# Kernel optimization log

Hardware: AMD Instinct MI355X
Metric: run time of the kernel (lower is better)

Reference implementation:

```python
import jax, jax.numpy as jnp
import numpy as np

B, L, SIZE, BACK, H = 4, 1024, 1024, 512, 16
D = SIZE // H  # head_size = 64


def setup_inputs() -> dict:
    key = jax.random.key(0)
    ks = jax.random.split(key, 18)
    s = 0.02
    return {
        "k": jax.random.normal(ks[0], (B, L, SIZE), jnp.float32),
        "v": jax.random.normal(ks[1], (B, L, SIZE), jnp.float32),
        "q": jax.random.normal(ks[2], (B, L, SIZE), jnp.float32),
        "background": jax.random.normal(ks[3], (B, L, BACK), jnp.float32),
        # weights stored [in, out] (pre-transposed vs torch Linear)
        "Wk": jax.random.normal(ks[4], (SIZE, SIZE), jnp.float32) * s,
        "bk": jnp.zeros((SIZE,), jnp.float32),
        "Wv": jax.random.normal(ks[5], (SIZE, SIZE), jnp.float32) * s,
        "bv": jnp.zeros((SIZE,), jnp.float32),
        "Wq": jax.random.normal(ks[6], (SIZE, SIZE), jnp.float32) * s,
        "bq": jnp.zeros((SIZE,), jnp.float32),
        "Wb": jax.random.normal(ks[7], (BACK, SIZE), jnp.float32) * s,
        "bb": jnp.zeros((SIZE,), jnp.float32),
        "Wo": jax.random.normal(ks[8], (SIZE, SIZE), jnp.float32) * s,
        "bo": jnp.zeros((SIZE,), jnp.float32),
    }


def _heads(x):
    # [B, L, H*D] -> [B, H, L, D]
    b, l, _ = x.shape
    return x.reshape(b, l, H, D).transpose(0, 2, 1, 3)


def reference(k, v, q, background, Wk, bk, Wv, bv, Wq, bq, Wb, bb, Wo, bo):
    kh = _heads(k @ Wk + bk)
    vh = _heads(v @ Wv + bv)
    qh = _heads(q @ Wq + bq) / jnp.sqrt(jnp.asarray(D, k.dtype))
    gh = _heads(background @ Wb + bb)
    scores = jnp.einsum("bhqd,bhkd->bhqk", qh, kh)   # [B,H,Lq,Lk]
    gates = jax.nn.sigmoid(jnp.einsum("bhqd,bhkd->bhqk", qh, gh))
    attn = jax.nn.softmax(scores, axis=-1) * gates    # dropout = identity (eval)
    ctx = jnp.einsum("bhqk,bhkd->bhqd", attn, vh)
    ctx = ctx.transpose(0, 2, 1, 3).reshape(k.shape[0], -1, H * D)
    return ctx @ Wo + bo
```

## Files before the change

### kernel.cpp

```cpp
#include <hip/hip_runtime.h>
#include <cstddef>
#include <cstdint>

typedef __attribute__((ext_vector_type(8))) short s16x8;
typedef __attribute__((ext_vector_type(4))) short s16x4;
typedef __attribute__((ext_vector_type(4))) float f32x4;
typedef __attribute__((ext_vector_type(4))) unsigned u32x4;

#define MFMA(a, b, c) __builtin_amdgcn_mfma_f32_16x16x32_bf16(a, b, c, 0, 0, 0)
#define LOG2E 1.44269504088896f

__device__ __forceinline__ short f2bf(float x) {
    uint32_t u = __float_as_uint(x);
    u = (u + 0x7FFFu + ((u >> 16) & 1u)) >> 16;
    return (short)u;
}

__device__ __forceinline__ void gld16(const void* g, void* l) {
    __builtin_amdgcn_global_load_lds(
        (const __attribute__((address_space(1))) unsigned int*)g,
        (__attribute__((address_space(3))) unsigned int*)l, 16, 0, 0);
}

__device__ __forceinline__ float fexp2(float x) {
#if __has_builtin(__builtin_amdgcn_exp2f)
    return __builtin_amdgcn_exp2f(x);
#else
    return exp2f(x);
#endif
}

__device__ __forceinline__ float frcp(float x) {
#if __has_builtin(__builtin_amdgcn_rcpf)
    return __builtin_amdgcn_rcpf(x);
#else
    return 1.f / x;
#endif
}

__device__ __forceinline__ unsigned cvtpk(float lo, float hi) {
    unsigned r;
    asm("v_cvt_pk_bf16_f32 %0, %1, %2" : "=v"(r) : "v"(lo), "v"(hi));
    return r;
}

struct WtP { const float* W[5]; short* Wt[5]; int K[5]; };

__global__ __launch_bounds__(256)
void conv_wt_b(WtP p) {
    __shared__ float T[64][65];
    const int z = blockIdx.z;
    const int K = p.K[z];
    const int k0 = blockIdx.y << 6, n0 = blockIdx.x << 6;
    if (k0 >= K) return;
    const float* W = p.W[z];
    short* Wt = p.Wt[z];
    const int tr = threadIdx.x >> 4, tc4 = (threadIdx.x & 15) << 2;
    #pragma unroll
    for (int i = 0; i < 4; ++i) {
        const int r = tr + i * 16;
        const float4 v = *(const float4*)(W + (size_t)(k0 + r) * 1024 + n0 + tc4);
        T[r][tc4 + 0] = v.x; T[r][tc4 + 1] = v.y;
        T[r][tc4 + 2] = v.z; T[r][tc4 + 3] = v.w;
    }
    __syncthreads();
    #pragma unroll
    for (int i = 0; i < 4; ++i) {
        const int nr = tr + i * 16;
        s16x4 o;
        o[0] = f2bf(T[tc4 + 0][nr]); o[1] = f2bf(T[tc4 + 1][nr]);
        o[2] = f2bf(T[tc4 + 2][nr]); o[3] = f2bf(T[tc4 + 3][nr]);
        *(s16x4*)(Wt + (size_t)(n0 + nr) * K + k0 + tc4) = o;
    }
}

struct Proj5P {
    const float* Af[5];
    const short* A[5];
    const short* Bt[5]; const float* bias[5];
    void* Y[5]; int Kd[5]; float alpha[5]; int mode[5];
};

__global__ __launch_bounds__(256, 2)
void proj_gemm128f(Proj5P p) {
    __shared__ __align__(16) short lds[2 * 16384];

    const int tid = threadIdx.x;
    const int w = tid >> 6, lane = tid & 63;
    const int la = lane & 15, kg = lane >> 4;
    const int wr = w >> 1, wc = w & 1;

    const int orig = blockIdx.x;
    const int swz = (orig & 7) * 128 + (orig >> 3);
    const int z = swz >> 8;
    const int rem = swz & 255;
    const int bm = rem >> 3, bn = rem & 7;

    const int K = p.Kd[z];
    const int NT = K >> 6;

    const int srow = tid >> 3;
    const int csrc = (tid & 7) ^ (srow & 7);
    const float* gAf = p.Af[z] + (size_t)(bm * 128 + srow) * K + csrc * 8;
    const short* gB  = p.Bt[z] + (size_t)(bn * 128 + srow) * K + csrc * 8;
    short* dstA = &lds[srow * 64 + (tid & 7) * 8];
    short* dstB = dstA + 8192;

    float4 av[4][2];

#define ISSUE_A(t) do {                                                    \
        const size_t ko_ = (size_t)((t) << 6);                             \
        _Pragma("unroll")                                                  \
        for (int i = 0; i < 4; ++i) {                                      \
            av[i][0] = *(const float4*)(gAf + (size_t)(32 * i) * K + ko_);     \
            av[i][1] = *(const float4*)(gAf + (size_t)(32 * i) * K + ko_ + 4); \
        }                                                                  \
    } while (0)
#define ISSUE_B(t, nb) do {                                                \
        const size_t ko_ = (size_t)((t) << 6);                             \
        _Pragma("unroll")                                                  \
        for (int i = 0; i < 4; ++i)                                        \
            gld16(gB + (size_t)(32 * i) * K + ko_,                         \
                  dstB + (nb) * 16384 + i * 2048);                         \
    } while (0)
#define A_WRITE(nb) do {                                                   \
        _Pragma("unroll")                                                  \
        for (int i = 0; i < 4; ++i) {                                      \
            u32x4 pk;                                                      \
            pk[0] = cvtpk(av[i][0].x, av[i][0].y);                         \
            pk[1] = cvtpk(av[i][0].z, av[i][0].w);                         \
            pk[2] = cvtpk(av[i][1].x, av[i][1].y);                         \
            pk[3] = cvtpk(av[i][1].z, av[i][1].w);                         \
            *(u32x4*)(dstA + (nb) * 16384 + i * 2048) = pk;                \
        }                                                                  \
    } while (0)

    const int c0 = kg ^ (la & 7), c1 = (4 + kg) ^ (la & 7);
    const int aRd = (wr * 64 + la) * 64;
    const int bRd = 8192 + (wc * 64 + la) * 64;

    f32x4 acc[4][4] = {};

    ISSUE_A(0);
    ISSUE_B(0, 0);
    A_WRITE(0);
    asm volatile("s_waitcnt vmcnt(0) lgkmcnt(0)" ::: "memory");
    asm volatile("s_barrier" ::: "memory");
    ISSUE_A(1);

    for (int t = 0; t < NT; ++t) {
        const int cb = (t & 1) * 16384;
        const int nbi = (t & 1) ^ 1;
        if (t + 1 < NT) ISSUE_B(t + 1, nbi);
        s16x8 af[4][2], bf[4][2];
        #pragma unroll
        for (int m = 0; m < 4; ++m) {
            af[m][0] = *(const s16x8*)&lds[cb + aRd + m * 1024 + c0 * 8];
            af[m][1] = *(const s16x8*)&lds[cb + aRd + m * 1024 + c1 * 8];
        }
        #pragma unroll
        for (int n = 0; n < 4; ++n) {
            bf[n][0] = *(const s16x8*)&lds[cb + bRd + n * 1024 + c0 * 8];
            bf[n][1] = *(const s16x8*)&lds[cb + bRd + n * 1024 + c1 * 8];
        }
        __builtin_amdgcn_s_setprio(1);
        #pragma unroll
        for (int m = 0; m < 4; ++m)
            #pragma unroll
            for (int n = 0; n < 4; ++n) {
                acc[m][n] = MFMA(af[m][0], bf[n][0], acc[m][n]);
                acc[m][n] = MFMA(af[m][1], bf[n][1], acc[m][n]);
            }
        __builtin_amdgcn_s_setprio(0);
        if (t + 1 < NT) {
            A_WRITE(nbi);
            if (t + 2 < NT) {
                ISSUE_A(t + 2);
                asm volatile("s_waitcnt vmcnt(8)" ::: "memory");
            } else {
                asm volatile("s_waitcnt vmcnt(0)" ::: "memory");
            }
            asm volatile("s_waitcnt lgkmcnt(0)" ::: "memory");
            asm volatile("s_barrier" ::: "memory");
        }
    }
#undef ISSUE_A
#undef ISSUE_B
#undef A_WRITE

    const float* __restrict__ bias = p.bias[z];
    const float alpha = p.alpha[z];
    const int mode = p.mode[z];

    if (mode == 2) {
        short* __restrict__ Y = (short*)p.Y[z];
        short* Tv = lds;
        asm volatile("s_waitcnt lgkmcnt(0)" ::: "memory");
        asm volatile("s_barrier" ::: "memory");
        #pragma unroll
        for (int ni = 0; ni < 4; ++ni) {
            const int rrow = wc * 64 + ni * 16 + la;
            const float bs = bias[bn * 128 + rrow];
            #pragma unroll
            for (int mi = 0; mi < 4; ++mi) {
                const int l0 = wr * 64 + mi * 16 + kg * 4;
                const unsigned d0 = cvtpk(alpha * (acc[mi][ni][0] + bs),
                                          alpha * (acc[mi][ni][1] + bs));
                const unsigned d1 = cvtpk(alpha * (acc[mi][ni][2] + bs),
                                          alpha * (acc[mi][ni][3] + bs));
                *(unsigned*)&Tv[rrow * 132 + l0]     = d0;
                *(unsigned*)&Tv[rrow * 132 + l0 + 2] = d1;
            }
        }
        asm volatile("s_waitcnt lgkmcnt(0)" ::: "memory");
        asm volatile("s_barrier" ::: "memory");
        const int bb_ = (bm * 128) >> 10;
        const int l0g = (bm * 128) & 1023;
        #pragma unroll
        for (int s = 0; s < 8; ++s) {
            const int c = tid + (s << 8);
            const int rr = c >> 4, seg = c & 15;
            const int hh = bn * 2 + (rr >> 6), dd = rr & 63;
            const s16x8 vv = *(const s16x8*)&Tv[rr * 132 + seg * 8];
            *(s16x8*)&Y[((((size_t)bb_ * 16 + hh) * 64 + dd) << 10) + l0g + seg * 8] = vv;
        }
        return;
    }

    #pragma unroll
    for (int n = 0; n < 4; ++n) {
        const int col = bn * 128 + wc * 64 + n * 16 + la;
        const float bs = bias[col];
        #pragma unroll
        for (int m = 0; m < 4; ++m) {
            const int row0 = bm * 128 + wr * 64 + m * 16 + kg * 4;
            #pragma unroll
            for (int r = 0; r < 4; ++r) {
                const float v = alpha * (acc[m][n][r] + bs);
                ((short*)p.Y[z])[(size_t)(row0 + r) * 1024 + col] = f2bf(v);
            }
        }
    }
}

__global__ __launch_bounds__(256, 3)
void proj_gemmO(Proj5P p) {
    __shared__ __align__(16) short lds[2 * 12288];

    const int tid = threadIdx.x;
    const int w = tid >> 6, lane = tid & 63;
    const int la = lane & 15, kg = lane >> 4;
    const int wr = w >> 1, wc = w & 1;

    const int orig = blockIdx.x;
    const int swz = (orig & 7) * 64 + (orig >> 3);
    const int bm = swz >> 4, bn = swz & 15;

    const int K = 1024, NT = 16;

    const int srow = tid >> 3;
    const int csrc = (tid & 7) ^ (srow & 7);
    const short* gA = p.A[4]  + (size_t)(bm * 128 + srow) * K + csrc * 8;
    const short* gB = p.Bt[4] + (size_t)(bn * 64 + srow) * K + csrc * 8;
    short* dstA = &lds[srow * 64 + (tid & 7) * 8];
    short* dstB = dstA + 8192;

#define STAGE(t, nb) do {                                                  \
        const size_t ko_ = (size_t)((t) << 6);                             \
        _Pragma("unroll")                                                  \
        for (int i = 0; i < 4; ++i)                                        \
            gld16(gA + (size_t)(32 * i) * K + ko_,                         \
                  dstA + (nb) * 12288 + i * 2048);                         \
        _Pragma("unroll")                                                  \
        for (int i = 0; i < 2; ++i)                                        \
            gld16(gB + (size_t)(32 * i) * K + ko_,                         \
                  dstB + (nb) * 12288 + i * 2048);                         \
    } while (0)

    const int c0 = kg ^ (la & 7), c1 = (4 + kg) ^ (la & 7);
    const int aRd = (wr * 64 + la) * 64;
    const int bRd = 8192 + (wc * 32 + la) * 64;

    f32x4 acc[4][2] = {};

    STAGE(0, 0);
    asm volatile("s_waitcnt vmcnt(0)" ::: "memory");
    asm volatile("s_barrier" ::: "memory");

    for (int t = 0; t < NT; ++t) {
        const int cb = (t & 1) * 12288;
        if (t + 1 < NT) STAGE(t + 1, (t & 1) ^ 1);
        s16x8 af[4][2], bf[2][2];
        #pragma unroll
        for (int m = 0; m < 4; ++m) {
            af[m][0] = *(const s16x8*)&lds[cb + aRd + m * 1024 + c0 * 8];
            af[m][1] = *(const s16x8*)&lds[cb + aRd + m * 1024 + c1 * 8];
        }
        #pragma unroll
        for (int n = 0; n < 2; ++n) {
            bf[n][0] = *(const s16x8*)&lds[cb + bRd + n * 1024 + c0 * 8];
            bf[n][1] = *(const s16x8*)&lds[cb + bRd + n * 1024 + c1 * 8];
        }
        __builtin_amdgcn_s_setprio(1);
        #pragma unroll
        for (int m = 0; m < 4; ++m)
            #pragma unroll
            for (int n = 0; n < 2; ++n) {
                acc[m][n] = MFMA(af[m][0], bf[n][0], acc[m][n]);
                acc[m][n] = MFMA(af[m][1], bf[n][1], acc[m][n]);
            }
        __builtin_amdgcn_s_setprio(0);
        if (t + 1 < NT) {
            asm volatile("s_waitcnt vmcnt(0)" ::: "memory");
            asm volatile("s_barrier" ::: "memory");
        }
    }
#undef STAGE

    const float* __restrict__ bias = p.bias[4];
    float* __restrict__ Y = (float*)p.Y[4];
    #pragma unroll
    for (int n = 0; n < 2; ++n) {
        const int col = bn * 64 + wc * 32 + n * 16 + la;
        const float bs = bias[col];
        #pragma unroll
        for (int m = 0; m < 4; ++m) {
            const int row0 = bm * 128 + wr * 64 + m * 16 + kg * 4;
            #pragma unroll
            for (int r = 0; r < 4; ++r)
                Y[(size_t)(row0 + r) * 1024 + col] = acc[m][n][r] + bs;
        }
    }
}

__global__ __launch_bounds__(512)
void attn_mfma(const short* __restrict__ qh, const short* __restrict__ kh,
               const short* __restrict__ gh, const short* __restrict__ vt,
               short* __restrict__ ctx) {
    __shared__ __align__(16) short lds[33792];

    const int tid = threadIdx.x, w = tid >> 6, lane = tid & 63;
    const int la = lane & 15, kg = lane >> 4;

    const int orig = blockIdx.x;
    const int xcd = orig & 7, i = orig >> 3;
    const int bh = xcd * 8 + (i >> 3);
    const int qt = i & 7;
    const int b = bh >> 4, h = bh & 15;
    const int q0 = qt << 7;

    const size_t hb = ((size_t)b << 20) + ((size_t)h << 6);
    const size_t vtbase = ((size_t)bh) << 16;

    const int qrow = q0 + w * 16 + la;
    const s16x8 aq0 = *(const s16x8*)(qh + hb + (size_t)qrow * 1024 + kg * 8);
    const s16x8 aq1 = *(const s16x8*)(qh + hb + (size_t)qrow * 1024 + 32 + kg * 8);

    const int sr = tid >> 3, sc = tid & 7;
    const int cs = sc ^ (sr & 7);
    const short* ksrc = kh + hb + (size_t)sr * 1024 + cs * 8;
    const short* gsrc = gh + hb + (size_t)sr * 1024 + cs * 8;
    const short* vsrc = vt + vtbase + (size_t)sr * 1024 + cs * 8;
    const int sdst = tid * 8;

    const int ch0 = (kg ^ (la & 7)) * 8;
    const int ch1 = ((4 + kg) ^ (la & 7)) * 8;
    const int pbase = 24576 + w * 1152;

    float s_run = 0.f;
    f32x4 o[4] = {};

#define ASTG(kt, bb) do {                                                  \
        const size_t kr_ = (size_t)((kt) << 6) * 1024;                     \
        gld16(ksrc + kr_, &lds[(bb) * 4096 + sdst]);                       \
        gld16(gsrc + kr_, &lds[8192 + (bb) * 4096 + sdst]);                \
        gld16(vsrc + ((kt) << 6), &lds[16384 + (bb) * 4096 + sdst]);       \
    } while (0)

    ASTG(0, 0);
    asm volatile("s_waitcnt vmcnt(0)" ::: "memory");
    asm volatile("s_barrier" ::: "memory");

    for (int kt = 0; kt < 16; ++kt) {
        const int cb = (kt & 1) * 4096;
        if (kt < 15) ASTG(kt + 1, (kt + 1) & 1);

        f32x4 st[4] = {}, gt[4] = {};
        #pragma unroll
        for (int nf = 0; nf < 4; ++nf) {
            const int rb = cb + (nf * 16 + la) * 64;
            const s16x8 kb0 = *(const s16x8*)&lds[rb + ch0];
            const s16x8 kb1 = *(const s16x8*)&lds[rb + ch1];
            st[nf] = MFMA(kb0, aq0, st[nf]);
            st[nf] = MFMA(kb1, aq1, st[nf]);
            const s16x8 gb0 = *(const s16x8*)&lds[8192 + rb + ch0];
            const s16x8 gb1 = *(const s16x8*)&lds[8192 + rb + ch1];
            gt[nf] = MFMA(gb0, aq0, gt[nf]);
            gt[nf] = MFMA(gb1, aq1, gt[nf]);
        }

        float ps = 0.f;
        unsigned pkw[4][2];
        #pragma unroll
        for (int nf = 0; nf < 4; ++nf) {
            const float p0 = fexp2(st[nf][0]);
            const float p1 = fexp2(st[nf][1]);
            const float p2 = fexp2(st[nf][2]);
            const float p3 = fexp2(st[nf][3]);
            ps += (p0 + p1) + (p2 + p3);
            const float g0 = frcp(1.f + fexp2(-gt[nf][0]));
            const float g1 = frcp(1.f + fexp2(-gt[nf][1]));
            const float g2 = frcp(1.f + fexp2(-gt[nf][2]));
            const float g3 = frcp(1.f + fexp2(-gt[nf][3]));
            pkw[nf][0] = cvtpk(p0 * g0, p1 * g1);
            pkw[nf][1] = cvtpk(p2 * g2, p3 * g3);
        }
        s_run += ps;

        #pragma unroll
        for (int nf = 0; nf < 4; ++nf) {
            *(unsigned*)&lds[pbase + la * 72 + nf * 16 + kg * 4]     = pkw[nf][0];
            *(unsigned*)&lds[pbase + la * 72 + nf * 16 + kg * 4 + 2] = pkw[nf][1];
        }

        const s16x8 pa0 = *(const s16x8*)&lds[pbase + la * 72 + kg * 8];
        const s16x8 pa1 = *(const s16x8*)&lds[pbase + la * 72 + 32 + kg * 8];
        #pragma unroll
        for (int nf = 0; nf < 4; ++nf) {
            const int rb = cb + (nf * 16 + la) * 64;
            const s16x8 vb0 = *(const s16x8*)&lds[16384 + rb + ch0];
            const s16x8 vb1 = *(const s16x8*)&lds[16384 + rb + ch1];
            o[nf] = MFMA(vb0, pa0, o[nf]);
            o[nf] = MFMA(vb1, pa1, o[nf]);
        }

        if (kt < 15) {
            asm volatile("s_waitcnt vmcnt(0)" ::: "memory");
            asm volatile("s_barrier" ::: "memory");
        }
    }
#undef ASTG

    float sv = s_run;
    sv += __shfl_xor(sv, 16);
    sv += __shfl_xor(sv, 32);
    const float inv = frcp(sv);
    short* crow = ctx + ((size_t)(b * 1024 + qrow) << 10) + (h << 6);
    #pragma unroll
    for (int nf = 0; nf < 4; ++nf) {
        *(unsigned*)(crow + nf * 16 + kg * 4)     = cvtpk(o[nf][0] * inv, o[nf][1] * inv);
        *(unsigned*)(crow + nf * 16 + kg * 4 + 2) = cvtpk(o[nf][2] * inv, o[nf][3] * inv);
    }
}

extern "C" void kernel_launch(void* const* d_in, const int* in_sizes, int n_in,
                              void* d_out, int out_size, void* d_ws, size_t ws_size,
                              hipStream_t stream) {
    (void)in_sizes; (void)n_in; (void)out_size; (void)ws_size;

    const float* k  = (const float*)d_in[0];
    const float* v  = (const float*)d_in[1];
    const float* q  = (const float*)d_in[2];
    const float* bg = (const float*)d_in[3];
    const float* Wk = (const float*)d_in[4];  const float* bk = (const float*)d_in[5];
    const float* Wv = (const float*)d_in[6];  const float* bv = (const float*)d_in[7];
    const float* Wq = (const float*)d_in[8];  const float* bq = (const float*)d_in[9];
    const float* Wb = (const float*)d_in[10]; const float* bb = (const float*)d_in[11];
    const float* Wo = (const float*)d_in[12]; const float* bo = (const float*)d_in[13];

    short* ws = (short*)d_ws;
    const size_t MN = (size_t)4096 * 1024;
    short* khb  = ws;
    short* qhb  = ws + MN;
    short* ghb  = ws + 2 * MN;
    short* vtb  = ws + 3 * MN;
    short* ctxb = ws + 4 * MN;
    short* wkt  = ws + 5 * MN;
    short* wvt  = wkt + 1048576;
    short* wqt  = wvt + 1048576;
    short* wot  = wqt + 1048576;
    short* wbt  = wot + 1048576;

    const dim3 blk(256);

    WtP wp;
    wp.W[0] = Wk; wp.Wt[0] = wkt; wp.K[0] = 1024;
    wp.W[1] = Wv; wp.Wt[1] = wvt; wp.K[1] = 1024;
    wp.W[2] = Wq; wp.Wt[2] = wqt; wp.K[2] = 1024;
    wp.W[3] = Wb; wp.Wt[3] = wbt; wp.K[3] = 512;
    wp.W[4] = Wo; wp.Wt[4] = wot; wp.K[4] = 1024;
    conv_wt_b<<<dim3(16, 16, 5), blk, 0, stream>>>(wp);

    Proj5P p5;
    p5.Af[0] = k;  p5.A[0] = nullptr; p5.Bt[0] = wkt; p5.bias[0] = bk;
    p5.Y[0] = khb; p5.Kd[0] = 1024; p5.alpha[0] = LOG2E;  p5.mode[0] = 0;
    p5.Af[1] = q;  p5.A[1] = nullptr; p5.Bt[1] = wqt; p5.bias[1] = bq;
    p5.Y[1] = qhb; p5.Kd[1] = 1024; p5.alpha[1] = 0.125f; p5.mode[1] = 0;
    p5.Af[2] = bg; p5.A[2] = nullptr; p5.Bt[2] = wbt; p5.bias[2] = bb;
    p5.Y[2] = ghb; p5.Kd[2] = 512;  p5.alpha[2] = LOG2E;  p5.mode[2] = 0;
    p5.Af[3] = v;  p5.A[3] = nullptr; p5.Bt[3] = wvt; p5.bias[3] = bv;
    p5.Y[3] = vtb; p5.Kd[3] = 1024; p5.alpha[3] = 1.0f;   p5.mode[3] = 2;
    p5.Af[4] = nullptr; p5.A[4] = ctxb; p5.Bt[4] = wot; p5.bias[4] = bo;
    p5.Y[4] = d_out; p5.Kd[4] = 1024; p5.alpha[4] = 1.0f; p5.mode[4] = 1;

    proj_gemm128f<<<dim3(1024), blk, 0, stream>>>(p5);
    attn_mfma<<<dim3(512), dim3(512), 0, stream>>>(qhb, khb, ghb, vtb, ctxb);
    proj_gemmO<<<dim3(512), blk, 0, stream>>>(p5);
}
```

Before: 106.6 us.

## Halve projection GEMM K-tile to 32 to double occupancy to four blocks per CU

Measured after the change: 192.2 us. 1.8x slower.

```diff
diff --git a/kernel.cpp b/kernel.cpp
--- a/kernel.cpp
+++ b/kernel.cpp
@@ -81,9 +81,9 @@
     void* Y[5]; int Kd[5]; float alpha[5]; int mode[5];
 };
 
-__global__ __launch_bounds__(256, 2)
+__global__ __launch_bounds__(256, 4)
 void proj_gemm128f(Proj5P p) {
-    __shared__ __align__(16) short lds[2 * 16384];
+    __shared__ __align__(16) short lds[2 * 8192];
 
     const int tid = threadIdx.x;
     const int w = tid >> 6, lane = tid & 63;
@@ -97,86 +97,87 @@
     const int bm = rem >> 3, bn = rem & 7;
 
     const int K = p.Kd[z];
-    const int NT = K >> 6;
-
-    const int srow = tid >> 3;
-    const int csrc = (tid & 7) ^ (srow & 7);
-    const float* gAf = p.Af[z] + (size_t)(bm * 128 + srow) * K + csrc * 8;
-    const short* gB  = p.Bt[z] + (size_t)(bn * 128 + srow) * K + csrc * 8;
-    short* dstA = &lds[srow * 64 + (tid & 7) * 8];
-    short* dstB = dstA + 8192;
-
-    float4 av[4][2];
+    const int NT = K >> 5;
+
+    const int arow = tid >> 1, ah = tid & 1;
+    const int xa = (arow >> 1) & 3;
+    const float* gAf = p.Af[z] + (size_t)(bm * 128 + arow) * K;
+    const int ac0 = (2 * ah) ^ xa, ac1 = (2 * ah + 1) ^ xa;
+    short* dstA = &lds[arow * 32 + ah * 16];
+
+    const int br0 = w * 32 + (lane >> 2);
+    const int bcc = lane & 3;
+    const int xb0 = (br0 >> 1) & 3, xb1 = ((br0 + 16) >> 1) & 3;
+    const short* gB0 = p.Bt[z] + (size_t)(bn * 128 + br0) * K + ((bcc ^ xb0) * 8);
+    const short* gB1 = p.Bt[z] + (size_t)(bn * 128 + br0 + 16) * K + ((bcc ^ xb1) * 8);
+    short* dstB0 = &lds[4096 + w * 1024 + lane * 8];
+    short* dstB1 = dstB0 + 512;
+
+    float4 av[2][2];
 
 #define ISSUE_A(t) do {                                                    \
-        const size_t ko_ = (size_t)((t) << 6);                             \
-        _Pragma("unroll")                                                  \
-        for (int i = 0; i < 4; ++i) {                                      \
-            av[i][0] = *(const float4*)(gAf + (size_t)(32 * i) * K + ko_);     \
-            av[i][1] = *(const float4*)(gAf + (size_t)(32 * i) * K + ko_ + 4); \
-        }                                                                  \
+        const size_t ko_ = (size_t)((t) << 5);                             \
+        av[0][0] = *(const float4*)(gAf + ko_ + ac0 * 8);                  \
+        av[0][1] = *(const float4*)(gAf + ko_ + ac0 * 8 + 4);              \
+        av[1][0] = *(const float4*)(gAf + ko_ + ac1 * 8);                  \
+        av[1][1] = *(const float4*)(gAf + ko_ + ac1 * 8 + 4);              \
     } while (0)
 #define ISSUE_B(t, nb) do {                                                \
-        const size_t ko_ = (size_t)((t) << 6);                             \
-        _Pragma("unroll")                                                  \
-        for (int i = 0; i < 4; ++i)                                        \
-            gld16(gB + (size_t)(32 * i) * K + ko_,                         \
-                  dstB + (nb) * 16384 + i * 2048);                         \
+        const size_t ko_ = (size_t)((t) << 5);                             \
+        gld16(gB0 + ko_, dstB0 + (nb) * 8192);                             \
+        gld16(gB1 + ko_, dstB1 + (nb) * 8192);                             \
     } while (0)
 #define A_WRITE(nb) do {                                                   \
-        _Pragma("unroll")                                                  \
-        for (int i = 0; i < 4; ++i) {                                      \
-            u32x4 pk;                                                      \
-            pk[0] = cvtpk(av[i][0].x, av[i][0].y);                         \
-            pk[1] = cvtpk(av[i][0].z, av[i][0].w);                         \
-            pk[2] = cvtpk(av[i][1].x, av[i][1].y);                         \
-            pk[3] = cvtpk(av[i][1].z, av[i][1].w);                         \
-            *(u32x4*)(dstA + (nb) * 16384 + i * 2048) = pk;                \
-        }                                                                  \
+        u32x4 pk0, pk1;                                                    \
+        pk0[0] = cvtpk(av[0][0].x, av[0][0].y);                            \
+        pk0[1] = cvtpk(av[0][0].z, av[0][0].w);                            \
+        pk0[2] = cvtpk(av[0][1].x, av[0][1].y);                            \
+        pk0[3] = cvtpk(av[0][1].z, av[0][1].w);                            \
+        pk1[0] = cvtpk(av[1][0].x, av[1][0].y);                            \
+        pk1[1] = cvtpk(av[1][0].z, av[1][0].w);                            \
+        pk1[2] = cvtpk(av[1][1].x, av[1][1].y);                            \
+        pk1[3] = cvtpk(av[1][1].z, av[1][1].w);                            \
+        *(u32x4*)(dstA + (nb) * 8192)     = pk0;                           \
+        *(u32x4*)(dstA + (nb) * 8192 + 8) = pk1;                           \
     } while (0)
-
-    const int c0 = kg ^ (la & 7), c1 = (4 + kg) ^ (la & 7);
-    const int aRd = (wr * 64 + la) * 64;
-    const int bRd = 8192 + (wc * 64 + la) * 64;
 
     f32x4 acc[4][4] = {};
 
     ISSUE_A(0);
     ISSUE_B(0, 0);
     A_WRITE(0);
-    asm volatile("s_waitcnt vmcnt(0) lgkmcnt(0)" ::: "memory");
+    ISSUE_A(1);
+    asm volatile("s_waitcnt vmcnt(4)" ::: "memory");
+    asm volatile("s_waitcnt lgkmcnt(0)" ::: "memory");
     asm volatile("s_barrier" ::: "memory");
-    ISSUE_A(1);
 
     for (int t = 0; t < NT; ++t) {
-        const int cb = (t & 1) * 16384;
+        const int cb = (t & 1) * 8192;
         const int nbi = (t & 1) ^ 1;
         if (t + 1 < NT) ISSUE_B(t + 1, nbi);
-        s16x8 af[4][2], bf[4][2];
+        s16x8 af[4], bf[4];
         #pragma unroll
         for (int m = 0; m < 4; ++m) {
-            af[m][0] = *(const s16x8*)&lds[cb + aRd + m * 1024 + c0 * 8];
-            af[m][1] = *(const s16x8*)&lds[cb + aRd + m * 1024 + c1 * 8];
+            const int row = wr * 64 + m * 16 + la;
+            af[m] = *(const s16x8*)&lds[cb + row * 32 + (kg ^ ((row >> 1) & 3)) * 8];
         }
         #pragma unroll
         for (int n = 0; n < 4; ++n) {
-            bf[n][0] = *(const s16x8*)&lds[cb + bRd + n * 1024 + c0 * 8];
-            bf[n][1] = *(const s16x8*)&lds[cb + bRd + n * 1024 + c1 * 8];
+            const int row = wc * 64 + n * 16 + la;
+            bf[n] = *(const s16x8*)&lds[cb + 4096 + row * 32 + (kg ^ ((row >> 1) & 3)) * 8];
         }
         __builtin_amdgcn_s_setprio(1);
         #pragma unroll
         for (int m = 0; m < 4; ++m)
             #pragma unroll
-            for (int n = 0; n < 4; ++n) {
-                acc[m][n] = MFMA(af[m][0], bf[n][0], acc[m][n]);
-                acc[m][n] = MFMA(af[m][1], bf[n][1], acc[m][n]);
-            }
+            for (int n = 0; n < 4; ++n)
+                acc[m][n] = MFMA(af[m], bf[n], acc[m][n]);
         __builtin_amdgcn_s_setprio(0);
         if (t + 1 < NT) {
             A_WRITE(nbi);
             if (t + 2 < NT) {
                 ISSUE_A(t + 2);
-                asm volatile("s_waitcnt vmcnt(8)" ::: "memory");
+                asm volatile("s_waitcnt vmcnt(4)" ::: "memory");
             } else {
                 asm volatile("s_waitcnt vmcnt(0)" ::: "memory");
             }
@@ -195,34 +196,39 @@
     if (mode == 2) {
         short* __restrict__ Y = (short*)p.Y[z];
         short* Tv = lds;
-        asm volatile("s_waitcnt lgkmcnt(0)" ::: "memory");
-        asm volatile("s_barrier" ::: "memory");
-        #pragma unroll
-        for (int ni = 0; ni < 4; ++ni) {
-            const int rrow = wc * 64 + ni * 16 + la;
-            const float bs = bias[bn * 128 + rrow];
-            #pragma unroll
-            for (int mi = 0; mi < 4; ++mi) {
-                const int l0 = wr * 64 + mi * 16 + kg * 4;
-                const unsigned d0 = cvtpk(alpha * (acc[mi][ni][0] + bs),
-                                          alpha * (acc[mi][ni][1] + bs));
-                const unsigned d1 = cvtpk(alpha * (acc[mi][ni][2] + bs),
-                                          alpha * (acc[mi][ni][3] + bs));
-                *(unsigned*)&Tv[rrow * 132 + l0]     = d0;
-                *(unsigned*)&Tv[rrow * 132 + l0 + 2] = d1;
-            }
-        }
-        asm volatile("s_waitcnt lgkmcnt(0)" ::: "memory");
-        asm volatile("s_barrier" ::: "memory");
         const int bb_ = (bm * 128) >> 10;
         const int l0g = (bm * 128) & 1023;
         #pragma unroll
-        for (int s = 0; s < 8; ++s) {
-            const int c = tid + (s << 8);
-            const int rr = c >> 4, seg = c & 15;
-            const int hh = bn * 2 + (rr >> 6), dd = rr & 63;
-            const s16x8 vv = *(const s16x8*)&Tv[rr * 132 + seg * 8];
-            *(s16x8*)&Y[((((size_t)bb_ * 16 + hh) * 64 + dd) << 10) + l0g + seg * 8] = vv;
+        for (int ph = 0; ph < 2; ++ph) {
+            asm volatile("s_waitcnt lgkmcnt(0)" ::: "memory");
+            asm volatile("s_barrier" ::: "memory");
+            if (wc == ph) {
+                #pragma unroll
+                for (int ni = 0; ni < 4; ++ni) {
+                    const int loc = ni * 16 + la;
+                    const float bs = bias[bn * 128 + ph * 64 + loc];
+                    #pragma unroll
+                    for (int mi = 0; mi < 4; ++mi) {
+                        const int l0 = wr * 64 + mi * 16 + kg * 4;
+                        const unsigned d0 = cvtpk(alpha * (acc[mi][ni][0] + bs),
+                                                  alpha * (acc[mi][ni][1] + bs));
+                        const unsigned d1 = cvtpk(alpha * (acc[mi][ni][2] + bs),
+                                                  alpha * (acc[mi][ni][3] + bs));
+                        *(unsigned*)&Tv[loc * 132 + l0]     = d0;
+                        *(unsigned*)&Tv[loc * 132 + l0 + 2] = d1;
+                    }
+                }
+            }
+            asm volatile("s_waitcnt lgkmcnt(0)" ::: "memory");
+            asm volatile("s_barrier" ::: "memory");
+            const int hh = bn * 2 + ph;
+            #pragma unroll
+            for (int s = 0; s < 4; ++s) {
+                const int c = tid + (s << 8);
+                const int loc = c >> 4, seg = c & 15;
+                const s16x8 vv = *(const s16x8*)&Tv[loc * 132 + seg * 8];
+                *(s16x8*)&Y[((((size_t)bb_ * 16 + hh) * 64 + loc) << 10) + l0g + seg * 8] = vv;
+            }
         }
         return;
     }
```
